# Kernel tuning notes

Measured on AMD Instinct MI355X. Metric: run time of the kernel, lower is better.

Reference implementation:

```python
import jax, jax.numpy as jnp
import numpy as np

N_EDGE_TYPES = 25
EF = 2  # edge feature dim (excluding type)
HID = 10


def _edge_nn(et, ef, emb, wh, bh, wg, bg):
    # y = relu(emb[et] * (ef@Wh+bh) + (ef@Wg+bg)) -> [E, in*out]
    return jax.nn.relu(emb[et] * (ef @ wh + bh) + (ef @ wg + bg))


def _nnconv(x, et, ef, src, dst, emb, wh, bh, wg, bg, root, bias, in_c, out_c):
    n = x.shape[0]
    w = _edge_nn(et, ef, emb, wh, bh, wg, bg).reshape(-1, in_c, out_c)  # [E,in,out]
    msg = jnp.einsum('ei,eio->eo', x[src], w)                          # per-edge matmul
    s = jax.ops.segment_sum(msg, dst, num_segments=n)
    cnt = jax.ops.segment_sum(jnp.ones((src.shape[0],), x.dtype), dst, num_segments=n)
    agg = s / jnp.maximum(cnt, 1.0)[:, None]                           # scatter-mean
    return agg + x @ root + bias


def _make_params(key, in_c, out_c):
    ks = jax.random.split(key, 6)
    d = in_c * out_c
    s = 0.1
    return dict(
        emb=jax.random.normal(ks[0], (N_EDGE_TYPES, d), jnp.float32) * s,
        wh=jax.random.normal(ks[1], (EF, d), jnp.float32) * s,
        bh=jax.random.normal(ks[2], (d,), jnp.float32) * s,
        wg=jax.random.normal(ks[3], (EF, d), jnp.float32) * s,
        bg=jax.random.normal(ks[4], (d,), jnp.float32) * s,
        root=jax.random.normal(ks[5], (in_c, out_c), jnp.float32) * s,
        bias=jnp.zeros((out_c,), jnp.float32),
    )


def setup_inputs() -> dict:
    key = jax.random.key(0)
    ks = jax.random.split(key, 12)
    N, E, IN_C, OUT_C, B = 50000, 250000, 16, 16, 8
    inp = {
        'x': jax.random.normal(ks[0], (N, IN_C), jnp.float32),
        'edge_feat': jax.random.normal(ks[1], (E, EF), jnp.float32),
        'edge_type': jax.random.randint(ks[2], (E,), 0, N_EDGE_TYPES),
        'edge_src': jax.random.randint(ks[3], (E,), 0, N),
        'edge_dst': jax.random.randint(ks[4], (E,), 0, N),
        'cell_type': jax.random.randint(ks[5], (N,), 0, 3),
        'batch_ids': jnp.sort(jax.random.randint(ks[6], (N,), 0, B)),
        'batch_size': B,
    }
    for i, (ic, oc) in enumerate([(IN_C, HID), (HID, HID), (HID, OUT_C)], start=1):
        p = _make_params(ks[6 + i], ic, oc)
        for k, v in p.items():
            inp[f'{k}{i}'] = v
    return inp


def reference(x, edge_feat,
              emb1, wh1, bh1, wg1, bg1, root1, bias1,
              emb2, wh2, bh2, wg2, bg2, root2, bias2,
              emb3, wh3, bh3, wg3, bg3, root3, bias3,
              edge_type, edge_src, edge_dst, cell_type, batch_ids, batch_size):
    in_c, out_c = x.shape[1], root3.shape[1]
    h = _nnconv(x, edge_type, edge_feat, edge_src, edge_dst,
                emb1, wh1, bh1, wg1, bg1, root1, bias1, in_c, HID)
    h = jax.nn.relu(h)  # dropout is identity in eval mode
    h = _nnconv(h, edge_type, edge_feat, edge_src, edge_dst,
                emb2, wh2, bh2, wg2, bg2, root2, bias2, HID, HID)
    h = jax.nn.relu(h)
    h = _nnconv(h, edge_type, edge_feat, edge_src, edge_dst,
                emb3, wh3, bh3, wg3, bg3, root3, bias3, HID, out_c)
    h = jax.nn.relu(h)
    # scatter-mean pooling over nodes with cell_type==1, grouped by graph id
    gate = (cell_type == 1).astype(jnp.int32)
    idx = gate * (batch_ids.astype(jnp.int32) + 1)  # 0 = discarded bucket
    nseg = batch_size + 1
    s = jax.ops.segment_sum(h, idx, num_segments=nseg)
    cnt = jax.ops.segment_sum(jnp.ones((h.shape[0],), h.dtype), idx, num_segments=nseg)
    pooled = s / jnp.maximum(cnt, 1.0)[:, None]
    return pooled[1:batch_size + 1, :]  # [B, out_c]
```

## Files before the change

kernel.cpp:

```cpp
#include <hip/hip_runtime.h>
#include <stdint.h>

#define IN1 16
#define HIDC 10
#define OUT3 16
#define NTYPES 25
#define MAXB 8
#define HSTR 12

#define D1 (IN1 * HIDC)
#define D2 (HIDC * HIDC)
#define D3 (HIDC * OUT3)

__global__ __launch_bounds__(256) void zero2_kernel(int* __restrict__ a, int na,
                                                    int* __restrict__ b, int nb) {
  int i = blockIdx.x * blockDim.x + threadIdx.x;
  int s = gridDim.x * blockDim.x;
  for (int j = i; j < na; j += s) a[j] = 0;
  for (int j = i; j < nb; j += s) b[j] = 0;
}

__global__ __launch_bounds__(256) void hist_kernel(const int* __restrict__ edst,
                                                   int* __restrict__ deg,
                                                   int* __restrict__ pos, int E) {
  int e = blockIdx.x * blockDim.x + threadIdx.x;
  if (e < E) pos[e] = atomicAdd(&deg[edst[e]], 1);
}

__global__ __launch_bounds__(256) void scan_part_kernel(const int* __restrict__ deg,
                                                        int* __restrict__ row_ptr,
                                                        int* __restrict__ bsum, int N) {
  __shared__ int wsums[4];
  int tid = threadIdx.x, lane = tid & 63, wid = tid >> 6;
  int idx0 = (blockIdx.x * 256 + tid) * 4;
  int4 v = make_int4(0, 0, 0, 0);
  if (idx0 < N)     v.x = deg[idx0];
  if (idx0 + 1 < N) v.y = deg[idx0 + 1];
  if (idx0 + 2 < N) v.z = deg[idx0 + 2];
  if (idx0 + 3 < N) v.w = deg[idx0 + 3];
  int s = v.x + v.y + v.z + v.w;
  int x = s;
  #pragma unroll
  for (int off = 1; off < 64; off <<= 1) {
    int y = __shfl_up(x, off);
    if (lane >= off) x += y;
  }
  if (lane == 63) wsums[wid] = x;
  __syncthreads();
  int wpre = 0;
  #pragma unroll
  for (int w = 0; w < 4; ++w) if (w < wid) wpre += wsums[w];
  int excl = x - s + wpre;
  if (idx0 < N)     row_ptr[idx0]     = excl;
  if (idx0 + 1 < N) row_ptr[idx0 + 1] = excl + v.x;
  if (idx0 + 2 < N) row_ptr[idx0 + 2] = excl + v.x + v.y;
  if (idx0 + 3 < N) row_ptr[idx0 + 3] = excl + v.x + v.y + v.z;
  if (tid == 255) bsum[blockIdx.x] = excl + s;
}

__global__ __launch_bounds__(64) void scan_bsum_kernel(int* __restrict__ bsum,
                                                       int* __restrict__ row_ptr,
                                                       int G, int N) {
  int tid = threadIdx.x;
  int v = (tid < G) ? bsum[tid] : 0;
  int x = v;
  #pragma unroll
  for (int off = 1; off < 64; off <<= 1) {
    int y = __shfl_up(x, off);
    if (tid >= off) x += y;
  }
  if (tid < G) bsum[tid] = x - v;
  if (tid == 63) row_ptr[N] = x;
}

__global__ __launch_bounds__(256) void scan_add_kernel(int* __restrict__ row_ptr,
                                                       const int* __restrict__ bsum,
                                                       int N) {
  int i = blockIdx.x * blockDim.x + threadIdx.x;
  if (i < N) row_ptr[i] += bsum[i >> 10];
}

__global__ __launch_bounds__(256) void permute_kernel(
    const int* __restrict__ edst, const int* __restrict__ esrc,
    const int* __restrict__ et, const float2* __restrict__ ef,
    const int* __restrict__ row_ptr, const int* __restrict__ pos,
    int4* __restrict__ edges, int E) {
  int e = blockIdx.x * blockDim.x + threadIdx.x;
  if (e >= E) return;
  int d = edst[e];
  int idx = row_ptr[d] + pos[e];
  float2 f = ef[e];
  int4 r;
  r.x = esrc[e];
  r.y = et[e];
  r.z = __float_as_int(f.x);
  r.w = __float_as_int(f.y);
  edges[idx] = r;
}

__global__ __launch_bounds__(256) void prep_kernel(
    const float* __restrict__ emb1, const float* __restrict__ wh1,
    const float* __restrict__ bh1, const float* __restrict__ wg1,
    const float* __restrict__ bg1,
    const float* __restrict__ emb2, const float* __restrict__ wh2,
    const float* __restrict__ bh2, const float* __restrict__ wg2,
    const float* __restrict__ bg2,
    const float* __restrict__ emb3, const float* __restrict__ wh3,
    const float* __restrict__ bh3, const float* __restrict__ wg3,
    const float* __restrict__ bg3,
    float4* __restrict__ P1, float4* __restrict__ P2, float4* __restrict__ P3)
{
  int i = blockIdx.x * 256 + threadIdx.x;
  const float *emb, *wh, *bh, *wg, *bg;
  float4* P; int D, k;
  if (i < NTYPES * D1) {
    emb = emb1; wh = wh1; bh = bh1; wg = wg1; bg = bg1; P = P1; D = D1; k = i;
  } else if (i < NTYPES * (D1 + D2)) {
    emb = emb2; wh = wh2; bh = bh2; wg = wg2; bg = bg2; P = P2; D = D2;
    k = i - NTYPES * D1;
  } else if (i < NTYPES * (D1 + D2 + D3)) {
    emb = emb3; wh = wh3; bh = bh3; wg = wg3; bg = bg3; P = P3; D = D3;
    k = i - NTYPES * (D1 + D2);
  } else return;
  int j = k - (k / D) * D;
  float e = emb[k];
  float4 p;
  p.x = fmaf(e, wh[j],     wg[j]);
  p.y = fmaf(e, wh[D + j], wg[D + j]);
  p.z = fmaf(e, bh[j],     bg[j]);
  p.w = 0.f;
  P[k] = p;
}

template<int IN_C, int O, int XS, bool POOL, int BS>
__global__ __launch_bounds__(BS) void layer_kernel(
    const float* __restrict__ xin,
    const int4* __restrict__ edges,
    const int* __restrict__ row_ptr,
    const float4* __restrict__ Pg,
    const float* __restrict__ root,
    const float* __restrict__ bias,
    float* __restrict__ hout,
    const int* __restrict__ ctype, const int* __restrict__ bids,
    float* __restrict__ pcnt,
    int N, int B)
{
  constexpr int D = IN_C * O;
  constexpr int NPB = BS / 16;
  __shared__ float4 s_P[NTYPES * D];
  __shared__ float s_psum[POOL ? (MAXB * 16) : 1];
  __shared__ float s_pcnt[POOL ? MAXB : 1];

  int tid = threadIdx.x;
  for (int k = tid; k < NTYPES * D; k += BS) s_P[k] = Pg[k];
  if (POOL) {
    for (int i = tid; i < MAXB * 16; i += BS) s_psum[i] = 0.f;
    for (int i = tid; i < MAXB; i += BS) s_pcnt[i] = 0.f;
  }
  __syncthreads();

  int nl = tid >> 4;
  int o = tid & 15;
  int oc = (O == 16) ? o : ((o < O) ? o : 0);
  int n = blockIdx.x * NPB + nl;

  float acc = 0.f;
  int start = 0, end = 0;
  if (n < N) { start = row_ptr[n]; end = row_ptr[n + 1]; }
  for (int e = start; e < end; ++e) {
    int4 r = edges[e];
    float f0 = __int_as_float(r.z), f1 = __int_as_float(r.w);
    const float4* __restrict__ pb = s_P + r.y * D + oc;
    const float* __restrict__ xr = xin + (size_t)r.x * XS;
    #pragma unroll
    for (int q = 0; q < IN_C / 4; ++q) {
      float4 xq = ((const float4*)xr)[q];
      float4 p0 = pb[(4 * q + 0) * O];
      float4 p1 = pb[(4 * q + 1) * O];
      float4 p2 = pb[(4 * q + 2) * O];
      float4 p3 = pb[(4 * q + 3) * O];
      acc = fmaf(xq.x, fmaxf(fmaf(f0, p0.x, fmaf(f1, p0.y, p0.z)), 0.f), acc);
      acc = fmaf(xq.y, fmaxf(fmaf(f0, p1.x, fmaf(f1, p1.y, p1.z)), 0.f), acc);
      acc = fmaf(xq.z, fmaxf(fmaf(f0, p2.x, fmaf(f1, p2.y, p2.z)), 0.f), acc);
      acc = fmaf(xq.w, fmaxf(fmaf(f0, p3.x, fmaf(f1, p3.y, p3.z)), 0.f), acc);
    }
    if constexpr (IN_C % 4 == 2) {
      float2 xq = ((const float2*)xr)[IN_C / 2 - 1];
      float4 p0 = pb[(IN_C - 2) * O];
      float4 p1 = pb[(IN_C - 1) * O];
      acc = fmaf(xq.x, fmaxf(fmaf(f0, p0.x, fmaf(f1, p0.y, p0.z)), 0.f), acc);
      acc = fmaf(xq.y, fmaxf(fmaf(f0, p1.x, fmaf(f1, p1.y, p1.z)), 0.f), acc);
    }
  }

  if (n < N && o < O) {
    float inv = 1.0f / fmaxf((float)(end - start), 1.0f);
    float v = fmaf(acc, inv, bias[o]);
    const float* __restrict__ xr = xin + (size_t)n * XS;
    #pragma unroll
    for (int i = 0; i < IN_C; ++i) v = fmaf(xr[i], root[i * O + o], v);
    v = fmaxf(v, 0.f);
    if (!POOL) {
      hout[(size_t)n * HSTR + o] = v;
    } else {
      if (ctype[n] == 1) {
        int b = bids[n];
        atomicAdd(&s_psum[b * 16 + o], v);
        if (o == 0) atomicAdd(&s_pcnt[b], 1.0f);
      }
    }
  }

  if (POOL) {
    __syncthreads();
    for (int i = tid; i < B * 16; i += BS) {
      float v = s_psum[i];
      if (v != 0.f) atomicAdd(&hout[i], v);
    }
    for (int i = tid; i < B; i += BS) {
      float c = s_pcnt[i];
      if (c != 0.f) atomicAdd(&pcnt[i], c);
    }
  }
}

__global__ __launch_bounds__(256) void finalize_kernel(
    const float* __restrict__ psum, const float* __restrict__ pcnt,
    float* __restrict__ out, int B) {
  int i = blockIdx.x * blockDim.x + threadIdx.x;
  if (i >= B * OUT3) return;
  int b = i / OUT3;
  out[i] = psum[i] / fmaxf(pcnt[b], 1.0f);
}

extern "C" void kernel_launch(void* const* d_in, const int* in_sizes, int n_in,
                              void* d_out, int out_size, void* d_ws, size_t ws_size,
                              hipStream_t stream)
{
  const float* x     = (const float*)d_in[0];
  const float* ef    = (const float*)d_in[1];
  const int*   et    = (const int*)d_in[2];
  const int*   esrc  = (const int*)d_in[3];
  const int*   edst  = (const int*)d_in[4];
  const int*   ctype = (const int*)d_in[5];
  const int*   bids  = (const int*)d_in[6];
  const float* emb1 = (const float*)d_in[8];
  const float* wh1  = (const float*)d_in[9];
  const float* bh1  = (const float*)d_in[10];
  const float* wg1  = (const float*)d_in[11];
  const float* bg1  = (const float*)d_in[12];
  const float* root1= (const float*)d_in[13];
  const float* bias1= (const float*)d_in[14];
  const float* emb2 = (const float*)d_in[15];
  const float* wh2  = (const float*)d_in[16];
  const float* bh2  = (const float*)d_in[17];
  const float* wg2  = (const float*)d_in[18];
  const float* bg2  = (const float*)d_in[19];
  const float* root2= (const float*)d_in[20];
  const float* bias2= (const float*)d_in[21];
  const float* emb3 = (const float*)d_in[22];
  const float* wh3  = (const float*)d_in[23];
  const float* bh3  = (const float*)d_in[24];
  const float* wg3  = (const float*)d_in[25];
  const float* bg3  = (const float*)d_in[26];
  const float* root3= (const float*)d_in[27];
  const float* bias3= (const float*)d_in[28];

  const int N = in_sizes[0] / IN1;
  const int E = in_sizes[2];
  const int B = out_size / OUT3;

  int4* edges   = (int4*)d_ws;
  int*  deg     = (int*)(edges + E);
  int*  pos     = deg + N;
  int*  row_ptr = pos + E;
  int*  bsum    = row_ptr + (N + 1);
  uintptr_t pp  = ((uintptr_t)(bsum + 64) + 15) & ~(uintptr_t)15;
  float4* P1    = (float4*)pp;
  float4* P2    = P1 + NTYPES * D1;
  float4* P3    = P2 + NTYPES * D2;
  float* h1     = (float*)(P3 + NTYPES * D3);
  float* h2     = h1 + (size_t)N * HSTR;
  float* psum   = h2 + (size_t)N * HSTR;
  float* pcnt   = psum + (size_t)B * 16;

  const int nChunk = (N + 1023) / 1024;
  const int nPrep  = NTYPES * (D1 + D2 + D3);

  zero2_kernel<<<128, 256, 0, stream>>>(deg, N, (int*)psum, B * 16 + B);
  prep_kernel<<<(nPrep + 255) / 256, 256, 0, stream>>>(
      emb1, wh1, bh1, wg1, bg1, emb2, wh2, bh2, wg2, bg2,
      emb3, wh3, bh3, wg3, bg3, P1, P2, P3);
  hist_kernel<<<(E + 255) / 256, 256, 0, stream>>>(edst, deg, pos, E);
  scan_part_kernel<<<nChunk, 256, 0, stream>>>(deg, row_ptr, bsum, N);
  scan_bsum_kernel<<<1, 64, 0, stream>>>(bsum, row_ptr, nChunk, N);
  scan_add_kernel<<<(N + 255) / 256, 256, 0, stream>>>(row_ptr, bsum, N);
  permute_kernel<<<(E + 255) / 256, 256, 0, stream>>>(
      edst, esrc, et, (const float2*)ef, row_ptr, pos, edges, E);

  const int g512 = (N + 31) / 32;
  layer_kernel<IN1, HIDC, IN1, false, 512><<<g512, 512, 0, stream>>>(
      x, edges, row_ptr, P1, root1, bias1,
      h1, nullptr, nullptr, nullptr, N, B);
  layer_kernel<HIDC, HIDC, HSTR, false, 512><<<g512, 512, 0, stream>>>(
      h1, edges, row_ptr, P2, root2, bias2,
      h2, nullptr, nullptr, nullptr, N, B);

  const int g1024 = (N + 63) / 64;
  layer_kernel<HIDC, OUT3, HSTR, true, 1024><<<g1024, 1024, 0, stream>>>(
      h2, edges, row_ptr, P3, root3, bias3,
      psum, ctype, bids, pcnt, N, B);

  finalize_kernel<<<1, 256, 0, stream>>>(psum, pcnt, (float*)d_out, B);
}
```

Measured before the change: 251.2 us.

## Fuse setup kernels, drop shared-memory P staging, fold finalize into last layer

Merges the zeroing and parameter-prep kernels into one grid-stride init kernel. The two-kernel block-sum scan becomes a single add kernel in which each block reduces its own prefix. The finalize pass moves into the last layer kernel through a last-block-done atomic counter. The layer kernels stop copying the per-type parameter table into LDS and read it from global memory (likely cache-resident), use smaller blocks for layers 1-2, and add an occupancy hint; this cuts launch count and LDS load time but risks more scattered global reads.

```diff
diff --git a/kernel.cpp b/kernel.cpp
--- a/kernel.cpp
+++ b/kernel.cpp
@@ -12,12 +12,48 @@
 #define D2 (HIDC * HIDC)
 #define D3 (HIDC * OUT3)
 
-__global__ __launch_bounds__(256) void zero2_kernel(int* __restrict__ a, int na,
-                                                    int* __restrict__ b, int nb) {
-  int i = blockIdx.x * blockDim.x + threadIdx.x;
-  int s = gridDim.x * blockDim.x;
-  for (int j = i; j < na; j += s) a[j] = 0;
-  for (int j = i; j < nb; j += s) b[j] = 0;
+__global__ __launch_bounds__(256) void init_kernel(
+    const float* __restrict__ emb1, const float* __restrict__ wh1,
+    const float* __restrict__ bh1, const float* __restrict__ wg1,
+    const float* __restrict__ bg1,
+    const float* __restrict__ emb2, const float* __restrict__ wh2,
+    const float* __restrict__ bh2, const float* __restrict__ wg2,
+    const float* __restrict__ bg2,
+    const float* __restrict__ emb3, const float* __restrict__ wh3,
+    const float* __restrict__ bh3, const float* __restrict__ wg3,
+    const float* __restrict__ bg3,
+    float4* __restrict__ P1, float4* __restrict__ P2, float4* __restrict__ P3,
+    int* __restrict__ deg, int N,
+    float* __restrict__ psum, float* __restrict__ pcnt,
+    int* __restrict__ done, int B)
+{
+  int gtid = blockIdx.x * 256 + threadIdx.x;
+  int gstr = gridDim.x * 256;
+  const int nPrep = NTYPES * (D1 + D2 + D3);
+  for (int i = gtid; i < nPrep; i += gstr) {
+    const float *emb, *wh, *bh, *wg, *bg; float4* P; int D, k;
+    if (i < NTYPES * D1) {
+      emb = emb1; wh = wh1; bh = bh1; wg = wg1; bg = bg1; P = P1; D = D1; k = i;
+    } else if (i < NTYPES * (D1 + D2)) {
+      emb = emb2; wh = wh2; bh = bh2; wg = wg2; bg = bg2; P = P2; D = D2;
+      k = i - NTYPES * D1;
+    } else {
+      emb = emb3; wh = wh3; bh = bh3; wg = wg3; bg = bg3; P = P3; D = D3;
+      k = i - NTYPES * (D1 + D2);
+    }
+    int j = k - (k / D) * D;
+    float e = emb[k];
+    float4 p;
+    p.x = fmaf(e, wh[j],     wg[j]);
+    p.y = fmaf(e, wh[D + j], wg[D + j]);
+    p.z = fmaf(e, bh[j],     bg[j]);
+    p.w = 0.f;
+    P[k] = p;
+  }
+  for (int i = gtid; i < N; i += gstr) deg[i] = 0;
+  for (int i = gtid; i < B * 16; i += gstr) psum[i] = 0.f;
+  for (int i = gtid; i < B; i += gstr) pcnt[i] = 0.f;
+  if (gtid == 0) *done = 0;
 }
 
 __global__ __launch_bounds__(256) void hist_kernel(const int* __restrict__ edst,
@@ -58,26 +94,26 @@
   if (tid == 255) bsum[blockIdx.x] = excl + s;
 }
 
-__global__ __launch_bounds__(64) void scan_bsum_kernel(int* __restrict__ bsum,
-                                                       int* __restrict__ row_ptr,
-                                                       int G, int N) {
-  int tid = threadIdx.x;
-  int v = (tid < G) ? bsum[tid] : 0;
-  int x = v;
+__global__ __launch_bounds__(256) void scan_add2_kernel(int* __restrict__ row_ptr,
+                                                        const int* __restrict__ bsum,
+                                                        int N, int chunks) {
+  __shared__ int s_off;
+  int c = blockIdx.x, tid = threadIdx.x;
+  if (tid < 64) {
+    int v = (tid < c) ? bsum[tid] : 0;
+    #pragma unroll
+    for (int off = 32; off >= 1; off >>= 1) v += __shfl_xor(v, off);
+    if (tid == 0) s_off = v;
+  }
+  __syncthreads();
+  int off = s_off;
+  int base = c * 1024 + tid * 4;
   #pragma unroll
-  for (int off = 1; off < 64; off <<= 1) {
-    int y = __shfl_up(x, off);
-    if (tid >= off) x += y;
-  }
-  if (tid < G) bsum[tid] = x - v;
-  if (tid == 63) row_ptr[N] = x;
-}
-
-__global__ __launch_bounds__(256) void scan_add_kernel(int* __restrict__ row_ptr,
-                                                       const int* __restrict__ bsum,
-                                                       int N) {
-  int i = blockIdx.x * blockDim.x + threadIdx.x;
-  if (i < N) row_ptr[i] += bsum[i >> 10];
+  for (int j = 0; j < 4; ++j) {
+    int idx = base + j;
+    if (idx < N) row_ptr[idx] += off;
+  }
+  if (c == chunks - 1 && tid == 0) row_ptr[N] = off + bsum[c];
 }
 
 __global__ __launch_bounds__(256) void permute_kernel(
@@ -98,42 +134,8 @@
   edges[idx] = r;
 }
 
-__global__ __launch_bounds__(256) void prep_kernel(
-    const float* __restrict__ emb1, const float* __restrict__ wh1,
-    const float* __restrict__ bh1, const float* __restrict__ wg1,
-    const float* __restrict__ bg1,
-    const float* __restrict__ emb2, const float* __restrict__ wh2,
-    const float* __restrict__ bh2, const float* __restrict__ wg2,
-    const float* __restrict__ bg2,
-    const float* __restrict__ emb3, const float* __restrict__ wh3,
-    const float* __restrict__ bh3, const float* __restrict__ wg3,
-    const float* __restrict__ bg3,
-    float4* __restrict__ P1, float4* __restrict__ P2, float4* __restrict__ P3)
-{
-  int i = blockIdx.x * 256 + threadIdx.x;
-  const float *emb, *wh, *bh, *wg, *bg;
-  float4* P; int D, k;
-  if (i < NTYPES * D1) {
-    emb = emb1; wh = wh1; bh = bh1; wg = wg1; bg = bg1; P = P1; D = D1; k = i;
-  } else if (i < NTYPES * (D1 + D2)) {
-    emb = emb2; wh = wh2; bh = bh2; wg = wg2; bg = bg2; P = P2; D = D2;
-    k = i - NTYPES * D1;
-  } else if (i < NTYPES * (D1 + D2 + D3)) {
-    emb = emb3; wh = wh3; bh = bh3; wg = wg3; bg = bg3; P = P3; D = D3;
-    k = i - NTYPES * (D1 + D2);
-  } else return;
-  int j = k - (k / D) * D;
-  float e = emb[k];
-  float4 p;
-  p.x = fmaf(e, wh[j],     wg[j]);
-  p.y = fmaf(e, wh[D + j], wg[D + j]);
-  p.z = fmaf(e, bh[j],     bg[j]);
-  p.w = 0.f;
-  P[k] = p;
-}
-
 template<int IN_C, int O, int XS, bool POOL, int BS>
-__global__ __launch_bounds__(BS) void layer_kernel(
+__global__ __launch_bounds__(BS, 8) void layer_kernel(
     const float* __restrict__ xin,
     const int4* __restrict__ edges,
     const int* __restrict__ row_ptr,
@@ -143,21 +145,21 @@
     float* __restrict__ hout,
     const int* __restrict__ ctype, const int* __restrict__ bids,
     float* __restrict__ pcnt,
+    int* __restrict__ done,
+    float* __restrict__ out,
     int N, int B)
 {
   constexpr int D = IN_C * O;
   constexpr int NPB = BS / 16;
-  __shared__ float4 s_P[NTYPES * D];
   __shared__ float s_psum[POOL ? (MAXB * 16) : 1];
   __shared__ float s_pcnt[POOL ? MAXB : 1];
 
   int tid = threadIdx.x;
-  for (int k = tid; k < NTYPES * D; k += BS) s_P[k] = Pg[k];
   if (POOL) {
     for (int i = tid; i < MAXB * 16; i += BS) s_psum[i] = 0.f;
     for (int i = tid; i < MAXB; i += BS) s_pcnt[i] = 0.f;
-  }
-  __syncthreads();
+    __syncthreads();
+  }
 
   int nl = tid >> 4;
   int o = tid & 15;
@@ -170,7 +172,7 @@
   for (int e = start; e < end; ++e) {
     int4 r = edges[e];
     float f0 = __int_as_float(r.z), f1 = __int_as_float(r.w);
-    const float4* __restrict__ pb = s_P + r.y * D + oc;
+    const float4* __restrict__ pb = Pg + r.y * D + oc;
     const float* __restrict__ xr = xin + (size_t)r.x * XS;
     #pragma unroll
     for (int q = 0; q < IN_C / 4; ++q) {
@@ -221,16 +223,20 @@
       float c = s_pcnt[i];
       if (c != 0.f) atomicAdd(&pcnt[i], c);
     }
-  }
-}
-
-__global__ __launch_bounds__(256) void finalize_kernel(
-    const float* __restrict__ psum, const float* __restrict__ pcnt,
-    float* __restrict__ out, int B) {
-  int i = blockIdx.x * blockDim.x + threadIdx.x;
-  if (i >= B * OUT3) return;
-  int b = i / OUT3;
-  out[i] = psum[i] / fmaxf(pcnt[b], 1.0f);
+    __threadfence();
+    __shared__ int s_last;
+    if (tid == 0) s_last = (atomicAdd(done, 1) == (int)gridDim.x - 1) ? 1 : 0;
+    __syncthreads();
+    if (s_last) {
+      for (int i = tid; i < B * 16; i += BS) {
+        float ps = __hip_atomic_load(&hout[i], __ATOMIC_RELAXED,
+                                     __HIP_MEMORY_SCOPE_AGENT);
+        float c  = __hip_atomic_load(&pcnt[i / 16], __ATOMIC_RELAXED,
+                                     __HIP_MEMORY_SCOPE_AGENT);
+        out[i] = ps / fmaxf(c, 1.0f);
+      }
+    }
+  }
 }
 
 extern "C" void kernel_launch(void* const* d_in, const int* in_sizes, int n_in,
@@ -275,7 +281,8 @@
   int*  pos     = deg + N;
   int*  row_ptr = pos + E;
   int*  bsum    = row_ptr + (N + 1);
-  uintptr_t pp  = ((uintptr_t)(bsum + 64) + 15) & ~(uintptr_t)15;
+  int*  done    = bsum + 64;
+  uintptr_t pp  = ((uintptr_t)(done + 4) + 15) & ~(uintptr_t)15;
   float4* P1    = (float4*)pp;
   float4* P2    = P1 + NTYPES * D1;
   float4* P3    = P2 + NTYPES * D2;
@@ -285,31 +292,26 @@
   float* pcnt   = psum + (size_t)B * 16;
 
   const int nChunk = (N + 1023) / 1024;
-  const int nPrep  = NTYPES * (D1 + D2 + D3);
-
-  zero2_kernel<<<128, 256, 0, stream>>>(deg, N, (int*)psum, B * 16 + B);
-  prep_kernel<<<(nPrep + 255) / 256, 256, 0, stream>>>(
+
+  init_kernel<<<128, 256, 0, stream>>>(
       emb1, wh1, bh1, wg1, bg1, emb2, wh2, bh2, wg2, bg2,
-      emb3, wh3, bh3, wg3, bg3, P1, P2, P3);
+      emb3, wh3, bh3, wg3, bg3, P1, P2, P3, deg, N, psum, pcnt, done, B);
   hist_kernel<<<(E + 255) / 256, 256, 0, stream>>>(edst, deg, pos, E);
   scan_part_kernel<<<nChunk, 256, 0, stream>>>(deg, row_ptr, bsum, N);
-  scan_bsum_kernel<<<1, 64, 0, stream>>>(bsum, row_ptr, nChunk, N);
-  scan_add_kernel<<<(N + 255) / 256, 256, 0, stream>>>(row_ptr, bsum, N);
+  scan_add2_kernel<<<nChunk, 256, 0, stream>>>(row_ptr, bsum, N, nChunk);
   permute_kernel<<<(E + 255) / 256, 256, 0, stream>>>(
       edst, esrc, et, (const float2*)ef, row_ptr, pos, edges, E);
 
-  const int g512 = (N + 31) / 32;
-  layer_kernel<IN1, HIDC, IN1, false, 512><<<g512, 512, 0, stream>>>(
+  const int g256 = (N + 15) / 16;
+  layer_kernel<IN1, HIDC, IN1, false, 256><<<g256, 256, 0, stream>>>(
       x, edges, row_ptr, P1, root1, bias1,
-      h1, nullptr, nullptr, nullptr, N, B);
-  layer_kernel<HIDC, HIDC, HSTR, false, 512><<<g512, 512, 0, stream>>>(
+      h1, nullptr, nullptr, nullptr, nullptr, nullptr, N, B);
+  layer_kernel<HIDC, HIDC, HSTR, false, 256><<<g256, 256, 0, stream>>>(
       h1, edges, row_ptr, P2, root2, bias2,
-      h2, nullptr, nullptr, nullptr, N, B);
+      h2, nullptr, nullptr, nullptr, nullptr, nullptr, N, B);
 
   const int g1024 = (N + 63) / 64;
   layer_kernel<HIDC, OUT3, HSTR, true, 1024><<<g1024, 1024, 0, stream>>>(
       h2, edges, row_ptr, P3, root3, bias3,
-      psum, ctype, bids, pcnt, N, B);
-
-  finalize_kernel<<<1, 256, 0, stream>>>(psum, pcnt, (float*)d_out, B);
-}
+      psum, ctype, bids, pcnt, done, (float*)d_out, N, B);
+}
```

Result: slower. 493.6 us (+96.5%).
